# Kernel tuning notes

Measured on AMD Instinct MI355X. Metric: run time of the kernel, lower is better.

Reference implementation:

```python
import jax, jax.numpy as jnp
import numpy as np

N, E, B = 30000, 300000, 64
F_N, F_E, F_G, H = 64, 32, 32, 64
EPS = 1e-5


def _bn(t, gamma, beta):
    # BatchNorm1d in training mode: biased batch statistics over the row dim.
    m = t.mean(axis=0)
    v = t.var(axis=0)
    return gamma * (t - m) * jax.lax.rsqrt(v + EPS) + beta


def _seg_mean(vals, idx, num):
    s = jax.ops.segment_sum(vals, idx, num_segments=num)
    c = jax.ops.segment_sum(jnp.ones((vals.shape[0], 1), vals.dtype), idx,
                            num_segments=num)
    return s / jnp.maximum(c, 1.0)


def setup_inputs() -> dict:
    key = jax.random.key(0)
    ks = jax.random.split(key, 32)
    inp = {
        'x': jax.random.normal(ks[0], (N, F_N), jnp.float32),
        'edge_index': jax.random.randint(ks[1], (2, E), 0, N),
        'e': jax.random.normal(ks[2], (E, F_E), jnp.float32),
        'u': jax.random.normal(ks[3], (B, F_G), jnp.float32),
        'batch': jnp.sort(jax.random.randint(ks[4], (N,), 0, B)),
        'g_node': jnp.ones((F_N,), jnp.float32),
        'b_node': jnp.zeros((F_N,), jnp.float32),
        'g_edge': jnp.ones((F_E,), jnp.float32),
        'b_edge': jnp.zeros((F_E,), jnp.float32),
        'g_glob': jnp.ones((F_G,), jnp.float32),
        'b_glob': jnp.zeros((F_G,), jnp.float32),
    }
    # Per-step Linear weights; input dims follow the feature-size threading in __init__.
    din_e = [2 * F_N + F_E + F_G, 3 * H + H, 3 * H + H]  # [192, 256, 256]
    din_n = [F_N + H + F_G, H + H + H, H + H + H]        # [160, 192, 192]
    din_g = [H + F_G, H + H, H + H]                      # [96, 128, 128]
    k = 5
    for l in range(3):
        for tag, din in (('e', din_e[l]), ('n', din_n[l]), ('g', din_g[l])):
            inp[f'W{tag}{l}'] = jax.random.normal(ks[k], (din, H), jnp.float32) / np.sqrt(din)
            inp[f'b{tag}{l}'] = jnp.zeros((H,), jnp.float32)
            k += 1
    return inp


def _forward(x, e, u, batch, src, dst,
             g_node, b_node, g_edge, b_edge, g_glob, b_glob,
             We, be, Wn, bn, Wg, bg):
    # Input normalization
    x = _bn(x, g_node, b_node)
    e = _bn(e, g_edge, b_edge)
    u = _bn(u, g_glob, b_glob)
    for l in range(3):
        # Edge model: per-edge MLP over [x_src, x_dst, e, u_edge]
        e_in = jnp.concatenate([x[src], x[dst], e, u[batch[src]]], axis=-1)
        e = jax.nn.relu(e_in @ We[l] + be[l])
        # Node model: aggregate incoming messages at destination (mean)
        agg = _seg_mean(e, dst, N)
        n_in = jnp.concatenate([x, agg, u[batch]], axis=-1)
        x = jax.nn.relu(n_in @ Wn[l] + bn[l])
        # Global model: mean-pool nodes per graph
        g_in = jnp.concatenate([_seg_mean(x, batch, B), u], axis=-1)
        u = jax.nn.relu(g_in @ Wg[l] + bg[l])
    return x, e, u


def reference(x, edge_index, e, u, batch,
              g_node, b_node, g_edge, b_edge, g_glob, b_glob,
              We0, be0, Wn0, bn0, Wg0, bg0,
              We1, be1, Wn1, bn1, Wg1, bg1,
              We2, be2, Wn2, bn2, Wg2, bg2):
    src, dst = edge_index[0], edge_index[1]
    We = (We0, We1, We2); be = (be0, be1, be2)
    Wn = (Wn0, Wn1, Wn2); bn = (bn0, bn1, bn2)
    Wg = (Wg0, Wg1, Wg2); bg = (bg0, bg1, bg2)
    return _forward(x, e, u, batch, src, dst,
                    g_node, b_node, g_edge, b_edge, g_glob, b_glob,
                    We, be, Wn, bn, Wg, bg)
```

## Files before the change

kernel.cpp:

```cpp
#include <hip/hip_runtime.h>
#include <hip/hip_bf16.h>

#define EPS 1e-5f
typedef __hip_bfloat16 bf16;
typedef __attribute__((ext_vector_type(8))) short  short8;
typedef __attribute__((ext_vector_type(4))) float  f32x4;

__device__ __forceinline__ float b2f(bf16 v) { return __bfloat162float(v); }
__device__ __forceinline__ float bs2f(short s) { bf16 b = *reinterpret_cast<bf16*>(&s); return b2f(b); }
__device__ __forceinline__ float ldv(const void* p, size_t i, bool bf) {
    return bf ? b2f(((const bf16*)p)[i]) : ((const float*)p)[i];
}
__device__ __forceinline__ void stv(void* p, size_t i, float v, bool bf) {
    if (bf) ((bf16*)p)[i] = __float2bfloat16(v);
    else    ((float*)p)[i] = v;
}
__device__ __forceinline__ short f2bs(float v) {
    bf16 b = __float2bfloat16(v);
    return *reinterpret_cast<short*>(&b);
}
__device__ __forceinline__ short8 ld16s(const short* p) { return *(const short8*)p; }

__global__ void detect_dtype(const unsigned short* __restrict__ xs, float* __restrict__ flag) {
    __shared__ int cnt;
    if (threadIdx.x == 0) cnt = 0;
    __syncthreads();
    unsigned short u = xs[threadIdx.x];
    int e = (u >> 7) & 0xFF;
    int sane = (u == 0 || (e >= 110 && e <= 140)) ? 1 : 0;
    atomicAdd(&cnt, sane);
    __syncthreads();
    if (threadIdx.x == 0) flag[0] = (cnt >= 230) ? 1.0f : 0.0f;
}

template<int C>
__global__ __launch_bounds__(256) void bn_stats(const void* __restrict__ in, int R,
                                                float* __restrict__ stats, const float* __restrict__ flag) {
    bool isbf = flag[0] != 0.f;
    const int RG = 256 / C;
    int c = threadIdx.x % C, rg = threadIdx.x / C;
    float s = 0.f, s2 = 0.f;
    if (isbf) {
        const bf16* ip = (const bf16*)in;
        for (int r = blockIdx.x * RG + rg; r < R; r += gridDim.x * RG) {
            float v = b2f(ip[(size_t)r * C + c]); s += v; s2 += v * v;
        }
    } else {
        const float* ip = (const float*)in;
        for (int r = blockIdx.x * RG + rg; r < R; r += gridDim.x * RG) {
            float v = ip[(size_t)r * C + c]; s += v; s2 += v * v;
        }
    }
    __shared__ float sm[2][256];
    sm[0][threadIdx.x] = s; sm[1][threadIdx.x] = s2;
    __syncthreads();
    if (threadIdx.x < C) {
        float ts = 0.f, t2 = 0.f;
        for (int g = 0; g < RG; g++) { ts += sm[0][g * C + c]; t2 += sm[1][g * C + c]; }
        atomicAdd(&stats[c], ts);
        atomicAdd(&stats[C + c], t2);
    }
}

__global__ __launch_bounds__(256) void bn_apply_x(const void* __restrict__ in, short* __restrict__ out,
                                                  const float* __restrict__ stats, int R,
                                                  const void* __restrict__ gamma, const void* __restrict__ beta,
                                                  const float* __restrict__ flag) {
    bool isbf = flag[0] != 0.f;
    int total = R * 64;
    for (int i = blockIdx.x * 256 + threadIdx.x; i < total; i += gridDim.x * 256) {
        int c = i & 63;
        float mean = stats[c] / (float)R;
        float var = stats[64 + c] / (float)R - mean * mean;
        float inv = rsqrtf(var + EPS);
        out[i] = f2bs(ldv(gamma, c, isbf) * (ldv(in, i, isbf) - mean) * inv + ldv(beta, c, isbf));
    }
}

__global__ __launch_bounds__(256) void bn_apply_u(const void* __restrict__ in, float* __restrict__ outf,
                                                  short* __restrict__ outb,
                                                  const float* __restrict__ stats, int R,
                                                  const void* __restrict__ gamma, const void* __restrict__ beta,
                                                  const float* __restrict__ flag) {
    bool isbf = flag[0] != 0.f;
    int total = R * 32;
    for (int i = blockIdx.x * 256 + threadIdx.x; i < total; i += gridDim.x * 256) {
        int c = i & 31;
        float mean = stats[c] / (float)R;
        float var = stats[32 + c] / (float)R - mean * mean;
        float inv = rsqrtf(var + EPS);
        float v = ldv(gamma, c, isbf) * (ldv(in, i, isbf) - mean) * inv + ldv(beta, c, isbf);
        outf[i] = v; outb[i] = f2bs(v);
    }
}

__global__ __launch_bounds__(256) void count_kernel(const int* __restrict__ ei, int* __restrict__ cnt, int E) {
    int stride = gridDim.x * 256;
    for (int t = blockIdx.x * 256 + threadIdx.x; t < E; t += stride) atomicAdd(&cnt[ei[E + t]], 1);
}

__global__ __launch_bounds__(256) void csr_offsets(const int* __restrict__ cnt, int* __restrict__ off,
                                                   int* __restrict__ wcur, int* __restrict__ cursor, int N,
                                                   const int* __restrict__ batch, int* __restrict__ gstart, int B) {
    int n = blockIdx.x * 256 + threadIdx.x;
    if (n < N) {
        int o = atomicAdd(cursor, cnt[n]);
        off[n] = o; wcur[n] = o;
    }
    if (blockIdx.x == 0 && threadIdx.x <= B) {
        int t = threadIdx.x;
        int lo = 0, hi = N;
        while (lo < hi) { int mid = (lo + hi) >> 1; if (batch[mid] < t) lo = mid + 1; else hi = mid; }
        gstart[t] = lo;
    }
}

__global__ __launch_bounds__(256) void csr_fill(const int* __restrict__ ei, int* __restrict__ wcur,
                                                int* __restrict__ csr, int E) {
    int stride = gridDim.x * 256;
    for (int t = blockIdx.x * 256 + threadIdx.x; t < E; t += stride) {
        int d = ei[E + t];
        int pos = atomicAdd(&wcur[d], 1);
        csr[pos] = t;
    }
}

__global__ __launch_bounds__(256) void transpose_w(
    const void* __restrict__ W0, const void* __restrict__ W1, const void* __restrict__ W2,
    const void* __restrict__ W3, const void* __restrict__ W4, const void* __restrict__ W5,
    short* __restrict__ out, const float* __restrict__ flag)
{
    bool isbf = flag[0] != 0.f;
    const void* Ws[6] = {W0, W1, W2, W3, W4, W5};
    const int   din[6] = {192, 256, 256, 160, 192, 192};
    int mtx = blockIdx.x >> 3;
    int off = 0;
    for (int i = 0; i < mtx; i++) off += 64 * din[i];
    int d = din[mtx];
    const void* W = Ws[mtx];
    for (int i = (blockIdx.x & 7) * 256 + threadIdx.x; i < 64 * d; i += 8 * 256) {
        int n = i / d, k = i % d;
        out[off + n * d + k] = f2bs(ldv(W, (size_t)k * 64 + n, isbf));
    }
}

template<bool L0>
__global__ __launch_bounds__(256) void edge_mfma(
    const int* __restrict__ ei, const int* __restrict__ batchv,
    const short* __restrict__ xb,
    const void* __restrict__ ein, size_t ein_off,
    const float* __restrict__ estats, const void* __restrict__ egamma, const void* __restrict__ ebeta,
    const short* __restrict__ ub,
    const short* __restrict__ Wt, const void* __restrict__ biasv,
    void* __restrict__ eout, size_t eout_off,
    int E, const float* __restrict__ flag,
    int ein_force_bf, int eout_force_bf, short* __restrict__ eout2)
{
    constexpr int DIN = L0 ? 192 : 256;
    constexpr int NQ = DIN / 32;
    constexpr int ROWB = DIN * 2;
    __shared__ __align__(16) char Wl[64 * ROWB];
    __shared__ __align__(16) char T[4 * 2048];
    const bool isbf = flag[0] != 0.f;
    const bool ein_bf = ein_force_bf ? true : isbf;
    const bool eout_bf = eout_force_bf ? true : isbf;
    const int w = threadIdx.x >> 6, j = threadIdx.x & 63;
    const int m16 = j & 15, c8v = j >> 4, c8 = c8v * 8;
    const int rr8 = j >> 3, cc8 = j & 7;

    for (int i = threadIdx.x; i < DIN * 8; i += 256) {
        int lin = i * 16;
        int row = i / (DIN / 8);
        *(short8*)(Wl + (lin ^ ((row & 7) << 4))) = *(const short8*)(Wt + i * 8);
    }
    __syncthreads();

    char* Tw = T + w * 2048;
    const int wkey = (m16 & 7) << 4;

    float sc[8], sh[8];
    if constexpr (L0) {
        #pragma unroll
        for (int k = 0; k < 8; k++) {
            int col = c8 + k;
            float m = estats[col] / (float)E;
            float iv = rsqrtf(estats[32 + col] / (float)E - m * m + EPS);
            sc[k] = ldv(egamma, col, isbf) * iv;
            sh[k] = ldv(ebeta, col, isbf) - m * sc[k];
        }
    }
    float bc[4];
    #pragma unroll
    for (int t = 0; t < 4; t++) bc[t] = ldv(biasv, t * 16 + m16, isbf);

    const int ntiles = (E + 63) >> 6;
    for (int tile = blockIdx.x; tile < ntiles; tile += gridDim.x) {
        const int we = tile * 64 + w * 16;
        int ec = we + m16; if (ec > E - 1) ec = E - 1;
        int s = ei[ec], d = ei[E + ec];
        int g = batchv[s];

        short8 af[NQ];
        af[0] = ld16s(xb + (size_t)s * 64 + c8);
        af[1] = ld16s(xb + (size_t)s * 64 + 32 + c8);
        af[2] = ld16s(xb + (size_t)d * 64 + c8);
        af[3] = ld16s(xb + (size_t)d * 64 + 32 + c8);
        if constexpr (L0) {
            float ev[8];
            if (isbf) {
                short8 r = ld16s((const short*)ein + (size_t)ec * 32 + c8);
                #pragma unroll
                for (int k = 0; k < 8; k++) ev[k] = bs2f(r[k]);
            } else {
                const float* ef = (const float*)ein + (size_t)ec * 32 + c8;
                float4 a = *(const float4*)ef, b = *(const float4*)(ef + 4);
                ev[0]=a.x; ev[1]=a.y; ev[2]=a.z; ev[3]=a.w; ev[4]=b.x; ev[5]=b.y; ev[6]=b.z; ev[7]=b.w;
            }
            #pragma unroll
            for (int k = 0; k < 8; k++) af[4][k] = f2bs(ev[k] * sc[k] + sh[k]);
            af[5] = ld16s(ub + (size_t)g * 32 + c8);
        } else {
            if (ein_bf) {
                af[4] = ld16s((const short*)ein + ein_off + (size_t)ec * 64 + c8);
                af[5] = ld16s((const short*)ein + ein_off + (size_t)ec * 64 + 32 + c8);
            } else {
                const float* ef = (const float*)ein + ein_off + (size_t)ec * 64;
                float4 a = *(const float4*)(ef + c8), b = *(const float4*)(ef + c8 + 4);
                af[4][0]=f2bs(a.x); af[4][1]=f2bs(a.y); af[4][2]=f2bs(a.z); af[4][3]=f2bs(a.w);
                af[4][4]=f2bs(b.x); af[4][5]=f2bs(b.y); af[4][6]=f2bs(b.z); af[4][7]=f2bs(b.w);
                a = *(const float4*)(ef + 32 + c8); b = *(const float4*)(ef + 36 + c8);
                af[5][0]=f2bs(a.x); af[5][1]=f2bs(a.y); af[5][2]=f2bs(a.z); af[5][3]=f2bs(a.w);
                af[5][4]=f2bs(b.x); af[5][5]=f2bs(b.y); af[5][6]=f2bs(b.z); af[5][7]=f2bs(b.w);
            }
            af[6] = ld16s(ub + (size_t)g * 64 + c8);
            af[7] = ld16s(ub + (size_t)g * 64 + 32 + c8);
        }

        f32x4 acc[4] = {{0,0,0,0},{0,0,0,0},{0,0,0,0},{0,0,0,0}};
        #pragma unroll
        for (int q = 0; q < NQ; q++) {
            #pragma unroll
            for (int t = 0; t < 4; t++) {
                int lin = (t * 16 + m16) * ROWB + q * 64 + c8v * 16;
                short8 bv = *(const short8*)(Wl + (lin ^ wkey));
                acc[t] = __builtin_amdgcn_mfma_f32_16x16x32_bf16(af[q], bv, acc[t], 0, 0, 0);
            }
        }

        #pragma unroll
        for (int t = 0; t < 4; t++) {
            #pragma unroll
            for (int r = 0; r < 4; r++) {
                float v = fmaxf(acc[t][r] + bc[t], 0.f);
                int rr = c8v * 4 + r;
                int lin = rr * 128 + (t * 16 + m16) * 2;
                *(short*)(Tw + (lin ^ ((rr & 7) << 4))) = f2bs(v);
            }
        }
        #pragma unroll
        for (int i = 0; i < 2; i++) {
            int r = i * 8 + rr8;
            int e2 = we + r;
            if (e2 < E) {
                short8 row = *(const short8*)(Tw + ((r * 128 + cc8 * 16) ^ ((rr8 & 7) << 4)));
                if (eout_bf) {
                    *(short8*)((short*)eout + eout_off + (size_t)e2 * 64 + cc8 * 8) = row;
                } else {
                    float* op = (float*)eout + eout_off + (size_t)e2 * 64 + cc8 * 8;
                    float4 a, b;
                    a.x=bs2f(row[0]); a.y=bs2f(row[1]); a.z=bs2f(row[2]); a.w=bs2f(row[3]);
                    b.x=bs2f(row[4]); b.y=bs2f(row[5]); b.z=bs2f(row[6]); b.w=bs2f(row[7]);
                    *(float4*)op = a; *(float4*)(op + 4) = b;
                }
                if (eout2) {
                    *(short8*)(eout2 + (size_t)e2 * 64 + cc8 * 8) = row;
                }
            }
        }
    }
}

template<bool L0, bool FINAL>
__global__ __launch_bounds__(256) void node_fused(
    const int* __restrict__ batchv, const short* __restrict__ xin,
    const int* __restrict__ off, const int* __restrict__ csr, const int* __restrict__ cntv,
    const void* __restrict__ eout, size_t eoff,
    const short* __restrict__ ub,
    const short* __restrict__ Wt, const void* __restrict__ biasv,
    short* __restrict__ xoutb, void* __restrict__ dout, int N,
    const float* __restrict__ flag, int e_force_bf)
{
    constexpr int DIN = L0 ? 160 : 192;
    constexpr int NQ = DIN / 32;
    constexpr int ROWB = DIN * 2;
    __shared__ __align__(16) char Wl[64 * ROWB];
    __shared__ __align__(16) char T[4 * 2048];
    const bool isbf = flag[0] != 0.f;
    const bool e_bf = e_force_bf ? true : isbf;
    const int w = threadIdx.x >> 6, j = threadIdx.x & 63;
    const int m16 = j & 15, c8v = j >> 4, c8 = c8v * 8;
    const int rr8 = j >> 3, cc8 = j & 7;
    const int nb = blockIdx.x * 64 + w * 16;

    for (int i = threadIdx.x; i < DIN * 8; i += 256) {
        int lin = i * 16;
        int row = i / (DIN / 8);
        *(short8*)(Wl + (lin ^ ((row & 7) << 4))) = *(const short8*)(Wt + i * 8);
    }
    __syncthreads();

    char* Tw = T + w * 2048;
    const int wkey = (m16 & 7) << 4;

    int n = nb + m16; if (n > N - 1) n = N - 1;
    int g = batchv[n];

    short8 af[NQ];
    af[0] = ld16s(xin + (size_t)n * 64 + c8);
    af[1] = ld16s(xin + (size_t)n * 64 + 32 + c8);

    {
        int st = off[n], c = cntv[n];
        float s0[8] = {0,0,0,0,0,0,0,0}, s1[8] = {0,0,0,0,0,0,0,0};
        int t = 0;
        if (e_bf) {
            const short* ep = (const short*)eout + eoff;
            for (; t + 2 <= c; t += 2) {
                int e0 = csr[st + t], e1 = csr[st + t + 1];
                short8 r0 = ld16s(ep + (size_t)e0 * 64 + c8);
                short8 q0 = ld16s(ep + (size_t)e0 * 64 + 32 + c8);
                short8 r1 = ld16s(ep + (size_t)e1 * 64 + c8);
                short8 q1 = ld16s(ep + (size_t)e1 * 64 + 32 + c8);
                #pragma unroll
                for (int k = 0; k < 8; k++) { s0[k] += bs2f(r0[k]) + bs2f(r1[k]); s1[k] += bs2f(q0[k]) + bs2f(q1[k]); }
            }
            if (t < c) {
                int e0 = csr[st + t];
                short8 r0 = ld16s(ep + (size_t)e0 * 64 + c8);
                short8 q0 = ld16s(ep + (size_t)e0 * 64 + 32 + c8);
                #pragma unroll
                for (int k = 0; k < 8; k++) { s0[k] += bs2f(r0[k]); s1[k] += bs2f(q0[k]); }
            }
        } else {
            const float* ep = (const float*)eout + eoff;
            for (; t < c; t++) {
                int e0 = csr[st + t];
                const float* rp = ep + (size_t)e0 * 64;
                float4 a = *(const float4*)(rp + c8), b = *(const float4*)(rp + c8 + 4);
                float4 x = *(const float4*)(rp + 32 + c8), y = *(const float4*)(rp + 36 + c8);
                s0[0]+=a.x; s0[1]+=a.y; s0[2]+=a.z; s0[3]+=a.w; s0[4]+=b.x; s0[5]+=b.y; s0[6]+=b.z; s0[7]+=b.w;
                s1[0]+=x.x; s1[1]+=x.y; s1[2]+=x.z; s1[3]+=x.w; s1[4]+=y.x; s1[5]+=y.y; s1[6]+=y.z; s1[7]+=y.w;
            }
        }
        float rc = 1.0f / fmaxf((float)c, 1.0f);
        #pragma unroll
        for (int k = 0; k < 8; k++) { af[2][k] = f2bs(s0[k] * rc); af[3][k] = f2bs(s1[k] * rc); }
    }

    if constexpr (L0) {
        af[4] = ld16s(ub + (size_t)g * 32 + c8);
    } else {
        af[4] = ld16s(ub + (size_t)g * 64 + c8);
        af[5] = ld16s(ub + (size_t)g * 64 + 32 + c8);
    }

    f32x4 acc[4] = {{0,0,0,0},{0,0,0,0},{0,0,0,0},{0,0,0,0}};
    #pragma unroll
    for (int q = 0; q < NQ; q++) {
        #pragma unroll
        for (int t = 0; t < 4; t++) {
            int lin = (t * 16 + m16) * ROWB + q * 64 + c8v * 16;
            short8 bv = *(const short8*)(Wl + (lin ^ wkey));
            acc[t] = __builtin_amdgcn_mfma_f32_16x16x32_bf16(af[q], bv, acc[t], 0, 0, 0);
        }
    }

    #pragma unroll
    for (int t = 0; t < 4; t++) {
        float bcv = ldv(biasv, t * 16 + m16, isbf);
        #pragma unroll
        for (int r = 0; r < 4; r++) {
            float v = fmaxf(acc[t][r] + bcv, 0.f);
            int rr = c8v * 4 + r;
            int lin = rr * 128 + (t * 16 + m16) * 2;
            *(short*)(Tw + (lin ^ ((rr & 7) << 4))) = f2bs(v);
        }
    }
    #pragma unroll
    for (int i = 0; i < 2; i++) {
        int r = i * 8 + rr8;
        int n2 = nb + r;
        if (n2 < N) {
            short8 row = *(const short8*)(Tw + ((r * 128 + cc8 * 16) ^ ((rr8 & 7) << 4)));
            *(short8*)&xoutb[(size_t)n2 * 64 + cc8 * 8] = row;
            if (FINAL) {
                if (isbf) {
                    *(short8*)((short*)dout + (size_t)n2 * 64 + cc8 * 8) = row;
                } else {
                    float* op = (float*)dout + (size_t)n2 * 64 + cc8 * 8;
                    float4 a, b;
                    a.x=bs2f(row[0]); a.y=bs2f(row[1]); a.z=bs2f(row[2]); a.w=bs2f(row[3]);
                    b.x=bs2f(row[4]); b.y=bs2f(row[5]); b.z=bs2f(row[6]); b.w=bs2f(row[7]);
                    *(float4*)op = a; *(float4*)(op + 4) = b;
                }
            }
        }
    }
}

__global__ __launch_bounds__(256) void pool_kernel(const int* __restrict__ gstart,
                                                   const short* __restrict__ xb,
                                                   float* __restrict__ gsum) {
    int g = blockIdx.x >> 3, slice = blockIdx.x & 7;
    int st = gstart[g], en = gstart[g + 1];
    int len = en - st;
    int K = (len + 7) >> 3;
    int b0 = st + slice * K;
    int b1 = min(b0 + K, en);
    int rg = threadIdx.x >> 3, cc8 = threadIdx.x & 7;
    float a[8] = {0,0,0,0,0,0,0,0};
    for (int r = b0 + rg; r < b1; r += 32) {
        short8 v = *(const short8*)&xb[(size_t)r * 64 + cc8 * 8];
        #pragma unroll
        for (int k = 0; k < 8; k++) a[k] += bs2f(v[k]);
    }
    __shared__ float sm[32][64];
    #pragma unroll
    for (int k = 0; k < 8; k++) sm[rg][cc8 * 8 + k] = a[k];
    __syncthreads();
    if (threadIdx.x < 64) {
        float s = 0.f;
        #pragma unroll 8
        for (int q = 0; q < 32; q++) s += sm[q][threadIdx.x];
        atomicAdd(&gsum[g * 64 + threadIdx.x], s);
    }
}

template<int FU>
__global__ __launch_bounds__(256) void glob_gemm(
    const int* __restrict__ gstart, const float* __restrict__ gsum,
    const float* __restrict__ uin,
    const void* __restrict__ W, const void* __restrict__ biasv,
    float* __restrict__ uoutf, short* __restrict__ uoutb,
    const float* __restrict__ flag)
{
    bool isbf = flag[0] != 0.f;
    const int DIN = 64 + FU;
    __shared__ float s[4][192];
    int w = threadIdx.x >> 6, j = threadIdx.x & 63;
    int g = blockIdx.x * 4 + w;
    int st = gstart[g], en = gstart[g + 1];
    float rc = 1.0f / fmaxf((float)(en - st), 1.0f);
    s[w][j] = gsum[g * 64 + j] * rc;
    if (j < FU) s[w][64 + j] = uin[g * FU + j];
    float acc = ldv(biasv, j, isbf);
    for (int k = 0; k < DIN; k++) acc += s[w][k] * ldv(W, (size_t)k * 64 + j, isbf);
    acc = fmaxf(acc, 0.f);
    uoutf[g * 64 + j] = acc;
    uoutb[g * 64 + j] = f2bs(acc);
}

__global__ __launch_bounds__(256) void cast_out(const float* __restrict__ in, void* __restrict__ out,
                                                size_t out_off, int n, const float* __restrict__ flag) {
    bool isbf = flag[0] != 0.f;
    for (int i = blockIdx.x * 256 + threadIdx.x; i < n; i += gridDim.x * 256)
        stv(out, out_off + i, in[i], isbf);
}

extern "C" void kernel_launch(void* const* d_in, const int* in_sizes, int n_in,
                              void* d_out, int out_size, void* d_ws, size_t ws_size,
                              hipStream_t stream) {
    const void* x_in   = d_in[0];
    const int*  ei     = (const int*)d_in[1];
    const void* e_raw  = d_in[2];
    const void* u_raw  = d_in[3];
    const int*  batchv = (const int*)d_in[4];
    const void *g_node = d_in[5],  *b_node = d_in[6];
    const void *g_edge = d_in[7],  *b_edge = d_in[8];
    const void *g_glob = d_in[9],  *b_glob = d_in[10];
    const void* We[3] = {d_in[11], d_in[17], d_in[23]};
    const void* be[3] = {d_in[12], d_in[18], d_in[24]};
    const void* Wn[3] = {d_in[13], d_in[19], d_in[25]};
    const void* bn[3] = {d_in[14], d_in[20], d_in[26]};
    const void* Wg[3] = {d_in[15], d_in[21], d_in[27]};
    const void* bg[3] = {d_in[16], d_in[22], d_in[28]};

    const int N = in_sizes[0] / 64;
    const int E = in_sizes[2] / 32;
    const int B = in_sizes[3] / 32;

    float* p = (float*)d_ws;
    float* zbase  = p;
    float* stats  = p; p += 3 * 128;
    int*   cursor = (int*)p; p += 4;
    int*   cnt    = (int*)p; p += N;
    float* gsum0  = p; p += B * 64;
    float* gsum1  = p; p += B * 64;
    float* gsum2  = p; p += B * 64;
    size_t zbytes = (size_t)((char*)p - (char*)zbase);
    float* dflag  = p; p += 4;
    float* uN     = p; p += B * 32;
    float* uA     = p; p += B * 64;
    float* uB     = p; p += B * 64;
    int*   off    = (int*)p; p += N;
    int*   wcur   = (int*)p; p += N;
    int*   gstart = (int*)p; p += 72;
    int*   csr    = (int*)p; p += E;
    short* xb0    = (short*)p; p += (size_t)N * 32;
    short* xb1    = (short*)p; p += (size_t)N * 32;
    short* ubN    = (short*)p; p += B * 16;
    short* ubA    = (short*)p; p += B * 32;
    short* ubB    = (short*)p; p += B * 32;
    short* WtAll  = (short*)p; p += 79872 / 2;
    const short* WtE0 = WtAll;
    const short* WtE1 = WtAll + 12288;
    const short* WtE2 = WtAll + 28672;
    const short* WtN0 = WtAll + 45056;
    const short* WtN1 = WtAll + 55296;
    const short* WtN2 = WtAll + 67584;

    short* eb16 = nullptr;
    {
        size_t used = (size_t)((char*)p - (char*)d_ws);
        used = (used + 15) & ~(size_t)15;
        size_t need = used + (size_t)E * 64 * sizeof(short);
        if (ws_size >= need) eb16 = (short*)((char*)d_ws + used);
    }

    const size_t EOFF = (size_t)N * 64;
    const size_t UOFF = EOFF + (size_t)E * 64;

    hipMemsetAsync(zbase, 0, zbytes, stream);

    detect_dtype<<<1, 256, 0, stream>>>((const unsigned short*)x_in, dflag);

    bn_stats<64><<<256, 256, 0, stream>>>(x_in, N, stats, dflag);
    bn_stats<32><<<512, 256, 0, stream>>>(e_raw, E, stats + 128, dflag);
    bn_stats<32><<<8,   256, 0, stream>>>(u_raw, B, stats + 256, dflag);
    bn_apply_x<<<512, 256, 0, stream>>>(x_in, xb0, stats, N, g_node, b_node, dflag);
    bn_apply_u<<<8,   256, 0, stream>>>(u_raw, uN, ubN, stats + 256, B, g_glob, b_glob, dflag);
    count_kernel<<<512, 256, 0, stream>>>(ei, cnt, E);
    csr_offsets<<<(N + 255) / 256, 256, 0, stream>>>(cnt, off, wcur, cursor, N, batchv, gstart, B);
    csr_fill<<<512, 256, 0, stream>>>(ei, wcur, csr, E);
    transpose_w<<<48, 256, 0, stream>>>(We[0], We[1], We[2], Wn[0], Wn[1], Wn[2], WtAll, dflag);

    const int NG = (N + 63) / 64;
    const int NT = (E + 63) / 64;
    const int EG0 = NT < 1280 ? NT : 1280;
    const int EG  = NT < 1024 ? NT : 1024;

    if (eb16) {
        edge_mfma<true><<<EG0, 256, 0, stream>>>(
            ei, batchv, xb0, e_raw, 0, stats + 128, g_edge, b_edge,
            ubN, WtE0, be[0], eb16, 0, E, dflag, 0, 1, nullptr);
        node_fused<true, false><<<NG, 256, 0, stream>>>(
            batchv, xb0, off, csr, cnt, eb16, 0, ubN, WtN0, bn[0], xb1, nullptr, N, dflag, 1);
        pool_kernel<<<B * 8, 256, 0, stream>>>(gstart, xb1, gsum0);
        glob_gemm<32><<<B / 4, 256, 0, stream>>>(gstart, gsum0, uN, Wg[0], bg[0], uA, ubA, dflag);

        edge_mfma<false><<<EG, 256, 0, stream>>>(
            ei, batchv, xb1, eb16, 0, nullptr, nullptr, nullptr,
            ubA, WtE1, be[1], eb16, 0, E, dflag, 1, 1, nullptr);
        node_fused<false, false><<<NG, 256, 0, stream>>>(
            batchv, xb1, off, csr, cnt, eb16, 0, ubA, WtN1, bn[1], xb0, nullptr, N, dflag, 1);
        pool_kernel<<<B * 8, 256, 0, stream>>>(gstart, xb0, gsum1);
        glob_gemm<64><<<B / 4, 256, 0, stream>>>(gstart, gsum1, uA, Wg[1], bg[1], uB, ubB, dflag);

        edge_mfma<false><<<EG, 256, 0, stream>>>(
            ei, batchv, xb0, eb16, 0, nullptr, nullptr, nullptr,
            ubB, WtE2, be[2], d_out, EOFF, E, dflag, 1, 0, eb16);
        node_fused<false, true><<<NG, 256, 0, stream>>>(
            batchv, xb0, off, csr, cnt, eb16, 0, ubB, WtN2, bn[2], xb1, d_out, N, dflag, 1);
        pool_kernel<<<B * 8, 256, 0, stream>>>(gstart, xb1, gsum2);
        glob_gemm<64><<<B / 4, 256, 0, stream>>>(gstart, gsum2, uB, Wg[2], bg[2], uA, ubA, dflag);
    } else {
        edge_mfma<true><<<EG0, 256, 0, stream>>>(
            ei, batchv, xb0, e_raw, 0, stats + 128, g_edge, b_edge,
            ubN, WtE0, be[0], d_out, EOFF, E, dflag, 0, 0, nullptr);
        node_fused<true, false><<<NG, 256, 0, stream>>>(
            batchv, xb0, off, csr, cnt, d_out, EOFF, ubN, WtN0, bn[0], xb1, nullptr, N, dflag, 0);
        pool_kernel<<<B * 8, 256, 0, stream>>>(gstart, xb1, gsum0);
        glob_gemm<32><<<B / 4, 256, 0, stream>>>(gstart, gsum0, uN, Wg[0], bg[0], uA, ubA, dflag);

        edge_mfma<false><<<EG, 256, 0, stream>>>(
            ei, batchv, xb1, d_out, EOFF, nullptr, nullptr, nullptr,
            ubA, WtE1, be[1], d_out, EOFF, E, dflag, 0, 0, nullptr);
        node_fused<false, false><<<NG, 256, 0, stream>>>(
            batchv, xb1, off, csr, cnt, d_out, EOFF, ubA, WtN1, bn[1], xb0, nullptr, N, dflag, 0);
        pool_kernel<<<B * 8, 256, 0, stream>>>(gstart, xb0, gsum1);
        glob_gemm<64><<<B / 4, 256, 0, stream>>>(gstart, gsum1, uA, Wg[1], bg[1], uB, ubB, dflag);

        edge_mfma<false><<<EG, 256, 0, stream>>>(
            ei, batchv, xb0, d_out, EOFF, nullptr, nullptr, nullptr,
            ubB, WtE2, be[2], d_out, EOFF, E, dflag, 0, 0, nullptr);
        node_fused<false, true><<<NG, 256, 0, stream>>>(
            batchv, xb0, off, csr, cnt, d_out, EOFF, ubB, WtN2, bn[2], xb1, d_out, N, dflag, 0);
        pool_kernel<<<B * 8, 256, 0, stream>>>(gstart, xb1, gsum2);
        glob_gemm<64><<<B / 4, 256, 0, stream>>>(gstart, gsum2, uB, Wg[2], bg[2], uA, ubA, dflag);
    }

    cast_out<<<16, 256, 0, stream>>>(uA, d_out, UOFF, B * 64, dflag);
}
```

Baseline: 478.3 us.

## Software-pipeline gathers in edge and node kernels and set occupancy launch bounds

The edge kernel now prefetches the next tile's indices and gathered x/e/u rows into registers while the current tile's MFMA and store run, with indices fetched two tiles ahead. The node kernel's CSR aggregation loop is restructured so edge-row loads for the next pair and indices for the pair after are issued before the current pair is accumulated. Both kernels also get a minimum-blocks-per-CU hint of 4. The aim is to hide gather latency behind compute, at the cost of higher register pressure that the occupancy hint may force into spills.

```diff
diff --git a/kernel.cpp b/kernel.cpp
--- a/kernel.cpp
+++ b/kernel.cpp
@@ -20,6 +20,13 @@
     return *reinterpret_cast<short*>(&b);
 }
 __device__ __forceinline__ short8 ld16s(const short* p) { return *(const short8*)p; }
+
+struct RawE {
+    short8 x0, x1, x2, x3;
+    short8 eA, eB;
+    float4 f0, f1, f2, f3;
+    short8 u0, u1;
+};
 
 __global__ void detect_dtype(const unsigned short* __restrict__ xs, float* __restrict__ flag) {
     __shared__ int cnt;
@@ -145,7 +152,7 @@
 }
 
 template<bool L0>
-__global__ __launch_bounds__(256) void edge_mfma(
+__global__ __launch_bounds__(256, 4) void edge_mfma(
     const int* __restrict__ ei, const int* __restrict__ batchv,
     const short* __restrict__ xb,
     const void* __restrict__ ein, size_t ein_off,
@@ -194,47 +201,87 @@
     for (int t = 0; t < 4; t++) bc[t] = ldv(biasv, t * 16 + m16, isbf);
 
     const int ntiles = (E + 63) >> 6;
-    for (int tile = blockIdx.x; tile < ntiles; tile += gridDim.x) {
-        const int we = tile * 64 + w * 16;
-        int ec = we + m16; if (ec > E - 1) ec = E - 1;
-        int s = ei[ec], d = ei[E + ec];
-        int g = batchv[s];
-
-        short8 af[NQ];
-        af[0] = ld16s(xb + (size_t)s * 64 + c8);
-        af[1] = ld16s(xb + (size_t)s * 64 + 32 + c8);
-        af[2] = ld16s(xb + (size_t)d * 64 + c8);
-        af[3] = ld16s(xb + (size_t)d * 64 + 32 + c8);
+    const int gs = gridDim.x;
+    int tile = blockIdx.x;
+    if (tile >= ntiles) return;
+
+    auto ldidx = [&](int t, int& s_, int& d_, int& ec_) {
+        int e_ = t * 64 + w * 16 + m16; if (e_ > E - 1) e_ = E - 1;
+        ec_ = e_; s_ = ei[e_]; d_ = ei[E + e_];
+    };
+    auto issue = [&](int s_, int d_, int ec_, int g_, RawE& R) {
+        R.x0 = ld16s(xb + (size_t)s_ * 64 + c8);
+        R.x1 = ld16s(xb + (size_t)s_ * 64 + 32 + c8);
+        R.x2 = ld16s(xb + (size_t)d_ * 64 + c8);
+        R.x3 = ld16s(xb + (size_t)d_ * 64 + 32 + c8);
+        if constexpr (L0) {
+            if (isbf) {
+                R.eA = ld16s((const short*)ein + (size_t)ec_ * 32 + c8);
+            } else {
+                const float* ef = (const float*)ein + (size_t)ec_ * 32 + c8;
+                R.f0 = *(const float4*)ef; R.f1 = *(const float4*)(ef + 4);
+            }
+            R.u0 = ld16s(ub + (size_t)g_ * 32 + c8);
+        } else {
+            if (ein_bf) {
+                R.eA = ld16s((const short*)ein + ein_off + (size_t)ec_ * 64 + c8);
+                R.eB = ld16s((const short*)ein + ein_off + (size_t)ec_ * 64 + 32 + c8);
+            } else {
+                const float* ef = (const float*)ein + ein_off + (size_t)ec_ * 64;
+                R.f0 = *(const float4*)(ef + c8);      R.f1 = *(const float4*)(ef + c8 + 4);
+                R.f2 = *(const float4*)(ef + 32 + c8); R.f3 = *(const float4*)(ef + 36 + c8);
+            }
+            R.u0 = ld16s(ub + (size_t)g_ * 64 + c8);
+            R.u1 = ld16s(ub + (size_t)g_ * 64 + 32 + c8);
+        }
+    };
+    auto fin = [&](const RawE& R, short8* af) {
+        af[0] = R.x0; af[1] = R.x1; af[2] = R.x2; af[3] = R.x3;
         if constexpr (L0) {
             float ev[8];
             if (isbf) {
-                short8 r = ld16s((const short*)ein + (size_t)ec * 32 + c8);
                 #pragma unroll
-                for (int k = 0; k < 8; k++) ev[k] = bs2f(r[k]);
+                for (int k = 0; k < 8; k++) ev[k] = bs2f(R.eA[k]);
             } else {
-                const float* ef = (const float*)ein + (size_t)ec * 32 + c8;
-                float4 a = *(const float4*)ef, b = *(const float4*)(ef + 4);
-                ev[0]=a.x; ev[1]=a.y; ev[2]=a.z; ev[3]=a.w; ev[4]=b.x; ev[5]=b.y; ev[6]=b.z; ev[7]=b.w;
+                ev[0]=R.f0.x; ev[1]=R.f0.y; ev[2]=R.f0.z; ev[3]=R.f0.w;
+                ev[4]=R.f1.x; ev[5]=R.f1.y; ev[6]=R.f1.z; ev[7]=R.f1.w;
             }
             #pragma unroll
             for (int k = 0; k < 8; k++) af[4][k] = f2bs(ev[k] * sc[k] + sh[k]);
-            af[5] = ld16s(ub + (size_t)g * 32 + c8);
+            af[5] = R.u0;
         } else {
-            if (ein_bf) {
-                af[4] = ld16s((const short*)ein + ein_off + (size_t)ec * 64 + c8);
-                af[5] = ld16s((const short*)ein + ein_off + (size_t)ec * 64 + 32 + c8);
-            } else {
-                const float* ef = (const float*)ein + ein_off + (size_t)ec * 64;
-                float4 a = *(const float4*)(ef + c8), b = *(const float4*)(ef + c8 + 4);
-                af[4][0]=f2bs(a.x); af[4][1]=f2bs(a.y); af[4][2]=f2bs(a.z); af[4][3]=f2bs(a.w);
-                af[4][4]=f2bs(b.x); af[4][5]=f2bs(b.y); af[4][6]=f2bs(b.z); af[4][7]=f2bs(b.w);
-                a = *(const float4*)(ef + 32 + c8); b = *(const float4*)(ef + 36 + c8);
-                af[5][0]=f2bs(a.x); af[5][1]=f2bs(a.y); af[5][2]=f2bs(a.z); af[5][3]=f2bs(a.w);
-                af[5][4]=f2bs(b.x); af[5][5]=f2bs(b.y); af[5][6]=f2bs(b.z); af[5][7]=f2bs(b.w);
-            }
-            af[6] = ld16s(ub + (size_t)g * 64 + c8);
-            af[7] = ld16s(ub + (size_t)g * 64 + 32 + c8);
-        }
+            if (ein_bf) { af[4] = R.eA; af[5] = R.eB; }
+            else {
+                af[4][0]=f2bs(R.f0.x); af[4][1]=f2bs(R.f0.y); af[4][2]=f2bs(R.f0.z); af[4][3]=f2bs(R.f0.w);
+                af[4][4]=f2bs(R.f1.x); af[4][5]=f2bs(R.f1.y); af[4][6]=f2bs(R.f1.z); af[4][7]=f2bs(R.f1.w);
+                af[5][0]=f2bs(R.f2.x); af[5][1]=f2bs(R.f2.y); af[5][2]=f2bs(R.f2.z); af[5][3]=f2bs(R.f2.w);
+                af[5][4]=f2bs(R.f3.x); af[5][5]=f2bs(R.f3.y); af[5][6]=f2bs(R.f3.z); af[5][7]=f2bs(R.f3.w);
+            }
+            af[6] = R.u0; af[7] = R.u1;
+        }
+    };
+
+    short8 af[NQ];
+    int sN = 0, dN = 0, ecN = 0;
+    {
+        RawE R;
+        int s0, d0, ec0;
+        ldidx(tile, s0, d0, ec0);
+        int g0 = batchv[s0];
+        issue(s0, d0, ec0, g0, R);
+        fin(R, af);
+        int t2 = tile + gs;
+        if (t2 < ntiles) ldidx(t2, sN, dN, ecN);
+    }
+
+    for (; tile < ntiles; tile += gs) {
+        const int tn = tile + gs;
+        const bool hasN = tn < ntiles;
+        RawE Rn; int gN = 0;
+        if (hasN) { gN = batchv[sN]; issue(sN, dN, ecN, gN, Rn); }
+        const int tnn = tn + gs;
+        int sQ = 0, dQ = 0, ecQ = 0;
+        if (tnn < ntiles) ldidx(tnn, sQ, dQ, ecQ);
 
         f32x4 acc[4] = {{0,0,0,0},{0,0,0,0},{0,0,0,0},{0,0,0,0}};
         #pragma unroll
@@ -247,6 +294,7 @@
             }
         }
 
+        const int we = tile * 64 + w * 16;
         #pragma unroll
         for (int t = 0; t < 4; t++) {
             #pragma unroll
@@ -277,11 +325,14 @@
                 }
             }
         }
+
+        if (hasN) fin(Rn, af);
+        if (tnn < ntiles) { sN = sQ; dN = dQ; ecN = ecQ; }
     }
 }
 
 template<bool L0, bool FINAL>
-__global__ __launch_bounds__(256) void node_fused(
+__global__ __launch_bounds__(256, 4) void node_fused(
     const int* __restrict__ batchv, const short* __restrict__ xin,
     const int* __restrict__ off, const int* __restrict__ csr, const int* __restrict__ cntv,
     const void* __restrict__ eout, size_t eoff,
@@ -322,20 +373,35 @@
     {
         int st = off[n], c = cntv[n];
         float s0[8] = {0,0,0,0,0,0,0,0}, s1[8] = {0,0,0,0,0,0,0,0};
-        int t = 0;
         if (e_bf) {
             const short* ep = (const short*)eout + eoff;
-            for (; t + 2 <= c; t += 2) {
-                int e0 = csr[st + t], e1 = csr[st + t + 1];
-                short8 r0 = ld16s(ep + (size_t)e0 * 64 + c8);
-                short8 q0 = ld16s(ep + (size_t)e0 * 64 + 32 + c8);
-                short8 r1 = ld16s(ep + (size_t)e1 * 64 + c8);
-                short8 q1 = ld16s(ep + (size_t)e1 * 64 + 32 + c8);
-                #pragma unroll
-                for (int k = 0; k < 8; k++) { s0[k] += bs2f(r0[k]) + bs2f(r1[k]); s1[k] += bs2f(q0[k]) + bs2f(q1[k]); }
-            }
-            if (t < c) {
-                int e0 = csr[st + t];
+            int npairs = c >> 1;
+            if (npairs > 0) {
+                int iA0 = csr[st], iA1 = csr[st + 1];
+                short8 rA0 = ld16s(ep + (size_t)iA0 * 64 + c8);
+                short8 qA0 = ld16s(ep + (size_t)iA0 * 64 + 32 + c8);
+                short8 rA1 = ld16s(ep + (size_t)iA1 * 64 + c8);
+                short8 qA1 = ld16s(ep + (size_t)iA1 * 64 + 32 + c8);
+                int aB = (1 < npairs) ? st + 2 : st;
+                int iB0 = csr[aB], iB1 = csr[aB + 1];
+                for (int p = 0; p < npairs; p++) {
+                    int aC = (p + 2 < npairs) ? st + 2 * (p + 2) : st;
+                    int iC0 = csr[aC], iC1 = csr[aC + 1];
+                    short8 rB0 = ld16s(ep + (size_t)iB0 * 64 + c8);
+                    short8 qB0 = ld16s(ep + (size_t)iB0 * 64 + 32 + c8);
+                    short8 rB1 = ld16s(ep + (size_t)iB1 * 64 + c8);
+                    short8 qB1 = ld16s(ep + (size_t)iB1 * 64 + 32 + c8);
+                    #pragma unroll
+                    for (int k = 0; k < 8; k++) {
+                        s0[k] += bs2f(rA0[k]) + bs2f(rA1[k]);
+                        s1[k] += bs2f(qA0[k]) + bs2f(qA1[k]);
+                    }
+                    rA0 = rB0; qA0 = qB0; rA1 = rB1; qA1 = qB1;
+                    iB0 = iC0; iB1 = iC1;
+                }
+            }
+            if (c & 1) {
+                int e0 = csr[st + c - 1];
                 short8 r0 = ld16s(ep + (size_t)e0 * 64 + c8);
                 short8 q0 = ld16s(ep + (size_t)e0 * 64 + 32 + c8);
                 #pragma unroll
@@ -343,7 +409,7 @@
             }
         } else {
             const float* ep = (const float*)eout + eoff;
-            for (; t < c; t++) {
+            for (int t = 0; t < c; t++) {
                 int e0 = csr[st + t];
                 const float* rp = ep + (size_t)e0 * 64;
                 float4 a = *(const float4*)(rp + c8), b = *(const float4*)(rp + c8 + 4);
```

Measured after the change: 845.0 us. +76.7%, slower.
